# Performance work log

Hardware: AMD Instinct MI355X
Metric: run time of the kernel (lower is better)

The kernel has to match this reference:

```python
import jax, jax.numpy as jnp
import numpy as np

B, S, C, D, V = 64, 128, 32, 512, 20000

def setup_inputs() -> dict:
    key = jax.random.key(0)
    ks = jax.random.split(key, 16)
    sc = 1.0 / np.sqrt(D)
    emb = jax.random.normal(ks[0], (V + 1, D), jnp.float32) * 0.02
    emb = emb.at[V].set(0.0)  # padding_idx=-1 -> last row zero
    inp = dict(
        emb=emb,
        W_all_w=jax.random.uniform(ks[1], (4 * D, D), jnp.float32, -sc, sc),
        W_all_b=jnp.zeros((4 * D,), jnp.float32),
        U_all_w=jax.random.uniform(ks[2], (4 * D, D), jnp.float32, -sc, sc),
        U_all_b=jnp.zeros((4 * D,), jnp.float32),
        W_d_w=jax.random.uniform(ks[3], (D, D), jnp.float32, -sc, sc),
        W_d_b=jnp.zeros((D,), jnp.float32),
        sel_w=jax.random.uniform(ks[4], (64, 1), jnp.float32, -1.0, 1.0),
        sel_b=jnp.zeros((64,), jnp.float32),
        time_w=jax.random.uniform(ks[5], (D, 64), jnp.float32, -0.125, 0.125),
        time_b=jnp.zeros((D,), jnp.float32),
        out_w=jax.random.uniform(ks[6], (2, D), jnp.float32, -sc, sc),
        out_b=jnp.zeros((2,), jnp.float32),
        seq_time_step=jax.random.uniform(ks[7], (B, S), jnp.float32, 0.0, 365.0),
        input_seqs=jax.random.randint(ks[8], (B, S, C), 0, V),
        mask=jnp.zeros((B, S), bool),
        lengths=jax.random.randint(ks[9], (B,), 1, S),
        codemask=jnp.zeros((B, S, C), bool),
        label=jax.random.randint(ks[10], (B,), 0, 2),
    )
    return inp


def reference(emb, W_all_w, W_all_b, U_all_w, U_all_b, W_d_w, W_d_b,
              sel_w, sel_b, time_w, time_b, out_w, out_b, seq_time_step,
              input_seqs, mask, lengths, codemask, label):
    # visit embedding: sum code embeddings -> [B,S,D]
    x = emb[input_seqs].sum(axis=2)
    # time feature: 1 - tanh(selection_layer(t/180)^2) -> time_layer -> [B,S,D]
    t = (seq_time_step / 180.0)[..., None]                      # [B,S,1]
    tf = 1.0 - jnp.tanh(jnp.square(t * sel_w[:, 0] + sel_b))    # [B,S,64]
    tf = jnp.einsum('bsk,dk->bsd', tf, time_w) + time_b         # [B,S,D]
    # precompute input projection for all steps: [B,S,4D]
    ux = jnp.einsum('bsd,ed->bse', x, U_all_w) + U_all_b

    def step(carry, inputs):
        h, c = carry
        tf_s, ux_s = inputs                                      # [B,D], [B,4D]
        c_s1 = jnp.tanh(c @ W_d_w.T + W_d_b)
        c_adj = c - c_s1 + c_s1 * tf_s
        outs = h @ W_all_w.T + W_all_b + ux_s
        f, i, o, c_tmp = jnp.split(jax.nn.sigmoid(outs), 4, axis=1)
        c_new = f * c_adj + i * c_tmp
        h_new = o * jnp.tanh(c_new)
        return (h_new, c_new), h_new

    h0 = jnp.zeros((B, D), x.dtype)
    c0 = jnp.zeros((B, D), x.dtype)
    tf_t = jnp.swapaxes(tf, 0, 1)   # [S,B,D]
    ux_t = jnp.swapaxes(ux, 0, 1)   # [S,B,4D]
    _, hs = jax.lax.scan(step, (h0, c0), (tf_t, ux_t))
    outputs = jnp.swapaxes(hs, 0, 1)           # [B,S,D]
    pooled = outputs.max(axis=1)                # MaxPoolLayer without mask
    out = pooled @ out_w.T + out_b              # [B,2]
    return out
```

## Files before the change

### kernel.cpp

```cpp
#include <hip/hip_runtime.h>
#include <hip/hip_bf16.h>

#define B_ 64
#define S_ 128
#define C_ 32
#define D_ 512
#define V_ 20000

typedef float     f32x4  __attribute__((ext_vector_type(4)));
typedef _Float16  f16x8  __attribute__((ext_vector_type(8)));

#define AS1 __attribute__((address_space(1)))
#define AS3 __attribute__((address_space(3)))

#define OFF_XH   0ull
#define OFF_UH   8388608ull
#define OFF_AW   10485760ull
#define OFF_CB   13631488ull
#define OFF_PAD  13639680ull
#define OFF_TWT  13647872ull
#define OFF_EMBH 13778944ull
#define OFF_TF   34259968ull
#define OFF_UX   42648576ull
#define OFF_XB2  76203008ull

#define SENT32 0x7FFF7FFFu

__global__ void k_prep_fused(
    const float* __restrict__ outb, float* __restrict__ outv,
    int4* __restrict__ fillp,
    const float* __restrict__ Wallb, const float* __restrict__ Uallb,
    float* __restrict__ cb,
    const float* __restrict__ tw, float* __restrict__ twt,
    const float* __restrict__ U, _Float16* __restrict__ uh,
    const float* __restrict__ Wall, const float* __restrict__ Wd,
    int4* __restrict__ AW,
    const float* __restrict__ emb, _Float16* __restrict__ eh)
{
    const int blk = blockIdx.x;
    const int t   = threadIdx.x;
    if (blk < 1) {
        if (t < 128) outv[t] = outb[t & 1];
    } else if (blk < 4097) {
        fillp[(blk - 1) * 256 + t] =
            int4{(int)SENT32, (int)SENT32, (int)SENT32, (int)SENT32};
    } else if (blk < 4098) {
        #pragma unroll
        for (int k = 0; k < 8; k++) {
            int i = t * 8 + k;
            cb[i] = Wallb[i] + Uallb[i];
        }
    } else if (blk < 4130) {
        int i2 = (blk - 4098) * 256 + t;
        #pragma unroll
        for (int k = 0; k < 4; k++) {
            int i = i2 * 4 + k;
            twt[(i & 63) * 512 + (i >> 6)] = tw[i];
        }
    } else if (blk < 5154) {
        int i = (blk - 4130) * 256 + t;
        float4 v = ((const float4*)U)[i];
        union { _Float16 h[4]; unsigned long long u; } pk;
        pk.h[0] = (_Float16)v.x; pk.h[1] = (_Float16)v.y;
        pk.h[2] = (_Float16)v.z; pk.h[3] = (_Float16)v.w;
        ((unsigned long long*)uh)[i] = pk.u;
    } else if (blk < 5922) {
        int i = (blk - 5154) * 256 + t;
        int lane = i & 63;  int r = i >> 6;
        int kt = r & 15;    r >>= 4;
        int tile = r % 3;   r /= 3;
        int w = r & 7;      int m = r >> 3;
        int row16 = lane & 15, quad = lane >> 4;
        int q = tile * 2 + (row16 >> 3);
        int d = m * 64 + w * 8 + (row16 & 7);
        int k0 = kt * 32 + quad * 8;
        union { _Float16 h[8]; int4 v; } u;
        const float* src = nullptr;
        if (q < 4)       src = Wall + (size_t)(q * 512 + d) * 512 + k0;
        else if (q == 4) src = Wd   + (size_t)d * 512 + k0;
        #pragma unroll
        for (int j = 0; j < 8; j++) u.h[j] = src ? (_Float16)src[j] : (_Float16)0.f;
        AW[i] = u.v;
    } else {
        int i = (blk - 5922) * 256 + t;
        float2 v = ((const float2*)emb)[i];
        unsigned short hx = __builtin_bit_cast(unsigned short, (_Float16)v.x);
        unsigned short hy = __builtin_bit_cast(unsigned short, (_Float16)v.y);
        ((unsigned*)eh)[i] = (unsigned)hx | ((unsigned)hy << 16);
    }
}

__global__ void k_embed2(const _Float16* __restrict__ embh, const int* __restrict__ seqs,
                         _Float16* __restrict__ xh)
{
    int bs = blockIdx.x;
    int t  = threadIdx.x;
    __shared__ int rows[32];
    if (t < 32) {
        int r = seqs[(size_t)bs * C_ + t];
        rows[t] = (r < 0) ? V_ : r;
    }
    __syncthreads();
    float ax = 0.f, ay = 0.f;
    #pragma unroll 4
    for (int c = 0; c < C_; c++) {
        unsigned v = *(const unsigned*)(embh + (size_t)rows[c] * D_ + 2 * t);
        ax += (float)__builtin_bit_cast(_Float16, (unsigned short)v);
        ay += (float)__builtin_bit_cast(_Float16, (unsigned short)(v >> 16));
    }
    unsigned short hx = __builtin_bit_cast(unsigned short, (_Float16)ax);
    unsigned short hy = __builtin_bit_cast(unsigned short, (_Float16)ay);
    *(unsigned*)(xh + (size_t)bs * D_ + 2 * t) = (unsigned)hx | ((unsigned)hy << 16);
}

__global__ __launch_bounds__(512) void k_tf2(
    const float* __restrict__ stime, const float* __restrict__ selw,
    const float* __restrict__ selb, const float* __restrict__ twT,
    const float* __restrict__ timeb, _Float16* __restrict__ tf)
{
    int bb = blockIdx.x;
    int t  = threadIdx.x;
    __shared__ float s1[16][64];
    for (int idx = t; idx < 1024; idx += 512) {
        int bl = idx >> 6, j = idx & 63;
        float tv = stime[bb * 16 + bl] * (1.0f / 180.0f);
        float u  = tv * selw[j] + selb[j];
        s1[bl][j] = 1.0f - tanhf(u * u);
    }
    __syncthreads();
    int d = t;
    float acc[16];
    float tb = timeb[d];
    #pragma unroll
    for (int l = 0; l < 16; l++) acc[l] = tb;
    for (int j = 0; j < 64; j++) {
        float wj = twT[j * 512 + d];
        #pragma unroll
        for (int l = 0; l < 16; l++) acc[l] = fmaf(s1[l][j], wj, acc[l]);
    }
    #pragma unroll
    for (int l = 0; l < 16; l++)
        tf[(size_t)(bb * 16 + l) * 512 + d] = (_Float16)acc[l];
}

__device__ __forceinline__ void stage16(const _Float16* g, _Float16* l)
{
#if __has_builtin(__builtin_amdgcn_global_load_lds)
    __builtin_amdgcn_global_load_lds((const AS1 void*)g, (AS3 void*)l, 16, 0, 0);
#else
    *(int4*)l = *(const int4*)g;
#endif
}

__global__ __launch_bounds__(256, 4) void k_gemm3(const _Float16* __restrict__ A,
                                                  const _Float16* __restrict__ Bm,
                                                  _Float16* __restrict__ Cg)
{
    __shared__ __align__(16) _Float16 As[128 * 64];
    __shared__ __align__(16) _Float16 Bs[128 * 64];
    const int t = threadIdx.x;
    const int w = t >> 6, lane = t & 63;
    const int wm = w & 1, wn = w >> 1;
    const int m0 = blockIdx.y * 128, n0 = blockIdx.x * 128;
    const int r16 = lane & 15, quad = lane >> 4;

    const int srow = w * 8 + (lane >> 3);
    const int k8g  = (lane & 7) ^ ((lane >> 3) & 7);
    const _Float16* ga = A  + (size_t)(m0 + srow) * 512 + k8g * 8;
    const _Float16* gb = Bm + (size_t)(n0 + srow) * 512 + k8g * 8;
    _Float16* la = As + srow * 64 + (lane & 7) * 8;
    _Float16* lb = Bs + srow * 64 + (lane & 7) * 8;

    f32x4 acc[4][4] = {};
    for (int k0 = 0; k0 < 512; k0 += 64) {
        __syncthreads();
        #pragma unroll
        for (int r = 0; r < 4; r++) {
            stage16(ga + k0 + (size_t)r * 32 * 512, la + r * 32 * 64);
            stage16(gb + k0 + (size_t)r * 32 * 512, lb + r * 32 * 64);
        }
        __syncthreads();
        #pragma unroll
        for (int sub = 0; sub < 2; sub++) {
            f16x8 af[4], bf[4];
            const int ksl = ((sub * 4 + quad) ^ (r16 & 7)) * 8;
            #pragma unroll
            for (int i = 0; i < 4; i++) {
                af[i] = *(const f16x8*)(As + (wm * 64 + i * 16 + r16) * 64 + ksl);
                bf[i] = *(const f16x8*)(Bs + (wn * 64 + i * 16 + r16) * 64 + ksl);
            }
            #pragma unroll
            for (int i = 0; i < 4; i++)
                #pragma unroll
                for (int j = 0; j < 4; j++)
                    acc[i][j] = __builtin_amdgcn_mfma_f32_16x16x32_f16(
                                    af[i], bf[j], acc[i][j], 0, 0, 0);
        }
    }
    #pragma unroll
    for (int i = 0; i < 4; i++)
        #pragma unroll
        for (int j = 0; j < 4; j++) {
            int row = m0 + wm * 64 + i * 16 + quad * 4;
            int col = n0 + wn * 64 + j * 16 + r16;
            _Float16* cp = Cg + (size_t)row * 2048 + col;
            #pragma unroll
            for (int rg = 0; rg < 4; rg++)
                cp[(size_t)rg * 2048] = (_Float16)acc[i][j][rg];
        }
}

__device__ __forceinline__ float fsigm(float x)
{
    return __builtin_amdgcn_rcpf(1.f + __expf(-x));
}
__device__ __forceinline__ float ftanh(float x)
{
    return 1.f - 2.f * __builtin_amdgcn_rcpf(1.f + __expf(2.f * x));
}

__global__ __launch_bounds__(512, 2) void k_rnn7(
    const int4* __restrict__ AW,
    const float* __restrict__ cbv, const float* __restrict__ wdb,
    const _Float16* __restrict__ ux, const _Float16* __restrict__ tf,
    const float* __restrict__ outw,
    float* __restrict__ out,
    unsigned long long* __restrict__ xb64)
{
    const int t    = threadIdx.x;
    const int gid  = blockIdx.x >> 3;
    const int m    = blockIdx.x & 7;
    const int b0   = gid * 2;
    const int w    = t >> 6;
    const int lane = t & 63;
    const int col  = lane & 15;
    const int quad = lane >> 4;

    int4 Af[48];
    {
        const int4* src = AW + (size_t)(m * 8 + w) * 3072;
        #pragma unroll
        for (int i = 0; i < 48; i++) Af[i] = src[i * 64 + lane];
    }

    __shared__ __align__(16) _Float16 xstg[4 * 544];
    __shared__ __align__(16) float cmat[8][4][48];
    __shared__ float pstg[2][64];

    const bool act = (lane < 16);
    const int  pb  = lane >> 3;
    const int  pj  = lane & 7;
    const int  dl  = w * 8 + pj;
    const int  d   = m * 64 + dl;

    float cbf = 0, cbi = 0, cbo = 0, cbc = 0, bdv = 0;
    if (act) {
        cbf = cbv[d]; cbi = cbv[512 + d]; cbo = cbv[1024 + d]; cbc = cbv[1536 + d];
        bdv = wdb[d];
    }
    float c_reg = 0.f, pool = -1e30f;
    const int dw = w * 64 + lane;

    for (int s = 0; s < S_; s++) {
        float uf = 0, ui = 0, uo = 0, uc = 0, tv = 0;
        if (act) {
            size_t bs = (size_t)(b0 + pb) * S_ + s;
            const _Float16* up = ux + bs * 2048 + d;
            uf = (float)up[0];    ui = (float)up[512];
            uo = (float)up[1024]; uc = (float)up[1536];
            tv = (float)tf[bs * 512 + d];
        }

        unsigned long long val = 0ull;
        if (s > 0) {
            const unsigned long long* src =
                xb64 + (((size_t)s * 32 + gid) * 8 + w) * 64 + lane;
            int tries = 0;
            for (;;) {
                val = __hip_atomic_load(src, __ATOMIC_RELAXED,
                                        __HIP_MEMORY_SCOPE_AGENT);
                if ((unsigned)val != SENT32 && (unsigned)(val >> 32) != SENT32)
                    break;
                if (++tries > (1 << 22)) break;
            }
        }
        __syncthreads();
        xstg[0 * 544 + dw] = __builtin_bit_cast(_Float16, (unsigned short)(val));
        xstg[2 * 544 + dw] = __builtin_bit_cast(_Float16, (unsigned short)(val >> 16));
        xstg[1 * 544 + dw] = __builtin_bit_cast(_Float16, (unsigned short)(val >> 32));
        xstg[3 * 544 + dw] = __builtin_bit_cast(_Float16, (unsigned short)(val >> 48));
        __syncthreads();

        f32x4 a0 = {0, 0, 0, 0}, a1 = {0, 0, 0, 0}, a2 = {0, 0, 0, 0};
        #pragma unroll
        for (int kt = 0; kt < 16; kt++) {
            f16x8 b = {};
            if (col < 4)
                b = *(const f16x8*)(xstg + col * 544 + kt * 32 + quad * 8);
            a0 = __builtin_amdgcn_mfma_f32_16x16x32_f16(
                     __builtin_bit_cast(f16x8, Af[kt]),      b, a0, 0, 0, 0);
            a1 = __builtin_amdgcn_mfma_f32_16x16x32_f16(
                     __builtin_bit_cast(f16x8, Af[16 + kt]), b, a1, 0, 0, 0);
            a2 = __builtin_amdgcn_mfma_f32_16x16x32_f16(
                     __builtin_bit_cast(f16x8, Af[32 + kt]), b, a2, 0, 0, 0);
        }

        if (col < 4) {
            *(f32x4*)&cmat[w][col][ 0 + quad * 4] = a0;
            *(f32x4*)&cmat[w][col][16 + quad * 4] = a1;
            *(f32x4*)&cmat[w][col][32 + quad * 4] = a2;
        }

        if (act) {
            float f_  = cmat[w][pb][ 0 + pj];
            float i_  = cmat[w][pb][ 8 + pj];
            float o_  = cmat[w][pb][16 + pj];
            float g_  = cmat[w][pb][24 + pj];
            float wd_ = cmat[w][2 + pb][32 + pj];
            float gf = fsigm(f_ + cbf + uf);
            float gi = fsigm(i_ + cbi + ui);
            float go = fsigm(o_ + cbo + uo);
            float gc = fsigm(g_ + cbc + uc);
            float cs1  = ftanh(wd_ + bdv);
            float cadj = c_reg - cs1 + cs1 * tv;
            float cn   = gf * cadj + gi * gc;
            float hn   = go * ftanh(cn);
            c_reg = cn;
            pool  = fmaxf(pool, hn);
            unsigned hh = __builtin_bit_cast(unsigned short, (_Float16)hn);
            unsigned cc = __builtin_bit_cast(unsigned short, (_Float16)cn);
            unsigned pk = hh | (cc << 16);
            unsigned other = __shfl(pk, lane + 8);
            if (pb == 0 && s != S_ - 1) {
                unsigned long long ov =
                    (unsigned long long)pk | ((unsigned long long)other << 32);
                unsigned long long* dst =
                    xb64 + (((size_t)(s + 1) * 32 + gid) * 8 + m) * 64 + dl;
                __hip_atomic_store(dst, ov, __ATOMIC_RELAXED,
                                   __HIP_MEMORY_SCOPE_AGENT);
            }
        }
    }

    if (act) pstg[pb][dl] = pool;
    __syncthreads();
    if (t < 128) {
        int b = t >> 6, l = t & 63;
        float pv = pstg[b][l];
        int dg = m * 64 + l;
        float p0 = pv * outw[dg], p1 = pv * outw[512 + dg];
        #pragma unroll
        for (int off = 32; off > 0; off >>= 1) {
            p0 += __shfl_down(p0, off);
            p1 += __shfl_down(p1, off);
        }
        if (l == 0) {
            atomicAdd(&out[2 * (b0 + b)],     p0);
            atomicAdd(&out[2 * (b0 + b) + 1], p1);
        }
    }
}

extern "C" void kernel_launch(void* const* d_in, const int* in_sizes, int n_in,
                              void* d_out, int out_size, void* d_ws, size_t ws_size,
                              hipStream_t stream)
{
    const float* emb   = (const float*)d_in[0];
    const float* Wall  = (const float*)d_in[1];
    const float* Wallb = (const float*)d_in[2];
    const float* Uall  = (const float*)d_in[3];
    const float* Uallb = (const float*)d_in[4];
    const float* Wdw   = (const float*)d_in[5];
    const float* Wdb   = (const float*)d_in[6];
    const float* selw  = (const float*)d_in[7];
    const float* selb  = (const float*)d_in[8];
    const float* timew = (const float*)d_in[9];
    const float* timeb = (const float*)d_in[10];
    const float* outw  = (const float*)d_in[11];
    const float* outb  = (const float*)d_in[12];
    const float* stime = (const float*)d_in[13];
    const int*   seqs  = (const int*)d_in[14];
    float* out = (float*)d_out;
    char*  ws  = (char*)d_ws;

    _Float16* xh   = (_Float16*)(ws + OFF_XH);
    _Float16* uh   = (_Float16*)(ws + OFF_UH);
    int4*     aw   = (int4*)(ws + OFF_AW);
    float*    cbp  = (float*)(ws + OFF_CB);
    float*    twt  = (float*)(ws + OFF_TWT);
    _Float16* eh   = (_Float16*)(ws + OFF_EMBH);
    _Float16* tfp  = (_Float16*)(ws + OFF_TF);
    _Float16* uxp  = (_Float16*)(ws + OFF_UX);
    unsigned long long* xb = (unsigned long long*)(ws + OFF_XB2);

    k_prep_fused<<<25923, 256, 0, stream>>>(
        outb, out, (int4*)(ws + OFF_XB2),
        Wallb, Uallb, cbp,
        timew, twt,
        Uall, uh,
        Wall, Wdw, aw,
        emb, eh);
    k_embed2 <<<B_ * S_, 256, 0, stream>>>(eh, seqs, xh);
    k_tf2    <<<512,     512, 0, stream>>>(stime, selw, selb, twt, timeb, tfp);
    k_gemm3  <<<dim3(16, 64), 256, 0, stream>>>(xh, uh, uxp);
    k_rnn7   <<<256,     512, 0, stream>>>(aw, cbp, Wdb, uxp, tfp, outw, out, xb);
}
```

Measured before the change: 471.1 us.

## Interleave two independent batch pairs per RNN block to hide cross-block latency

Each recurrent block now handles four batch rows as two independent pairs, alternating phases between them, so one pair's MFMA and gate work can proceed while the other pair's hidden state from peer blocks is still in flight. The grid is halved to 128 blocks, and the exchange buffer is reindexed per pair. This targets the spin-wait latency of the cross-block handoff, at the cost of twice as many serial phases per block and fewer resident blocks.

```diff
diff --git a/kernel.cpp b/kernel.cpp
--- a/kernel.cpp
+++ b/kernel.cpp
@@ -219,7 +219,7 @@
     return 1.f - 2.f * __builtin_amdgcn_rcpf(1.f + __expf(2.f * x));
 }
 
-__global__ __launch_bounds__(512, 2) void k_rnn7(
+__global__ __launch_bounds__(512, 2) void k_rnn8(
     const int4* __restrict__ AW,
     const float* __restrict__ cbv, const float* __restrict__ wdb,
     const _Float16* __restrict__ ux, const _Float16* __restrict__ tf,
@@ -230,7 +230,7 @@
     const int t    = threadIdx.x;
     const int gid  = blockIdx.x >> 3;
     const int m    = blockIdx.x & 7;
-    const int b0   = gid * 2;
+    const int b0   = gid * 4;
     const int w    = t >> 6;
     const int lane = t & 63;
     const int col  = lane & 15;
@@ -243,9 +243,9 @@
         for (int i = 0; i < 48; i++) Af[i] = src[i * 64 + lane];
     }
 
-    __shared__ __align__(16) _Float16 xstg[4 * 544];
+    __shared__ __align__(16) _Float16 xstg[2][4 * 544];
     __shared__ __align__(16) float cmat[8][4][48];
-    __shared__ float pstg[2][64];
+    __shared__ float pstg[4][64];
 
     const bool act = (lane < 16);
     const int  pb  = lane >> 3;
@@ -258,13 +258,17 @@
         cbf = cbv[d]; cbi = cbv[512 + d]; cbo = cbv[1024 + d]; cbc = cbv[1536 + d];
         bdv = wdb[d];
     }
-    float c_reg = 0.f, pool = -1e30f;
+    float c_reg[2] = {0.f, 0.f};
+    float pool[2]  = {-1e30f, -1e30f};
     const int dw = w * 64 + lane;
 
-    for (int s = 0; s < S_; s++) {
+    for (int ph = 0; ph < 2 * S_; ph++) {
+        const int pair = ph & 1;
+        const int s    = ph >> 1;
+
         float uf = 0, ui = 0, uo = 0, uc = 0, tv = 0;
         if (act) {
-            size_t bs = (size_t)(b0 + pb) * S_ + s;
+            size_t bs = (size_t)(b0 + pair * 2 + pb) * S_ + s;
             const _Float16* up = ux + bs * 2048 + d;
             uf = (float)up[0];    ui = (float)up[512];
             uo = (float)up[1024]; uc = (float)up[1536];
@@ -274,7 +278,7 @@
         unsigned long long val = 0ull;
         if (s > 0) {
             const unsigned long long* src =
-                xb64 + (((size_t)s * 32 + gid) * 8 + w) * 64 + lane;
+                xb64 + ((((size_t)s * 2 + pair) * 16 + gid) * 8 + w) * 64 + lane;
             int tries = 0;
             for (;;) {
                 val = __hip_atomic_load(src, __ATOMIC_RELAXED,
@@ -285,24 +289,30 @@
             }
         }
         __syncthreads();
-        xstg[0 * 544 + dw] = __builtin_bit_cast(_Float16, (unsigned short)(val));
-        xstg[2 * 544 + dw] = __builtin_bit_cast(_Float16, (unsigned short)(val >> 16));
-        xstg[1 * 544 + dw] = __builtin_bit_cast(_Float16, (unsigned short)(val >> 32));
-        xstg[3 * 544 + dw] = __builtin_bit_cast(_Float16, (unsigned short)(val >> 48));
+        {
+            _Float16* xs = xstg[pair];
+            xs[0 * 544 + dw] = __builtin_bit_cast(_Float16, (unsigned short)(val));
+            xs[2 * 544 + dw] = __builtin_bit_cast(_Float16, (unsigned short)(val >> 16));
+            xs[1 * 544 + dw] = __builtin_bit_cast(_Float16, (unsigned short)(val >> 32));
+            xs[3 * 544 + dw] = __builtin_bit_cast(_Float16, (unsigned short)(val >> 48));
+        }
         __syncthreads();
 
         f32x4 a0 = {0, 0, 0, 0}, a1 = {0, 0, 0, 0}, a2 = {0, 0, 0, 0};
-        #pragma unroll
-        for (int kt = 0; kt < 16; kt++) {
-            f16x8 b = {};
-            if (col < 4)
-                b = *(const f16x8*)(xstg + col * 544 + kt * 32 + quad * 8);
-            a0 = __builtin_amdgcn_mfma_f32_16x16x32_f16(
-                     __builtin_bit_cast(f16x8, Af[kt]),      b, a0, 0, 0, 0);
-            a1 = __builtin_amdgcn_mfma_f32_16x16x32_f16(
-                     __builtin_bit_cast(f16x8, Af[16 + kt]), b, a1, 0, 0, 0);
-            a2 = __builtin_amdgcn_mfma_f32_16x16x32_f16(
-                     __builtin_bit_cast(f16x8, Af[32 + kt]), b, a2, 0, 0, 0);
+        {
+            const _Float16* xs = xstg[pair];
+            #pragma unroll
+            for (int kt = 0; kt < 16; kt++) {
+                f16x8 b = {};
+                if (col < 4)
+                    b = *(const f16x8*)(xs + col * 544 + kt * 32 + quad * 8);
+                a0 = __builtin_amdgcn_mfma_f32_16x16x32_f16(
+                         __builtin_bit_cast(f16x8, Af[kt]),      b, a0, 0, 0, 0);
+                a1 = __builtin_amdgcn_mfma_f32_16x16x32_f16(
+                         __builtin_bit_cast(f16x8, Af[16 + kt]), b, a1, 0, 0, 0);
+                a2 = __builtin_amdgcn_mfma_f32_16x16x32_f16(
+                         __builtin_bit_cast(f16x8, Af[32 + kt]), b, a2, 0, 0, 0);
+            }
         }
 
         if (col < 4) {
@@ -322,11 +332,11 @@
             float go = fsigm(o_ + cbo + uo);
             float gc = fsigm(g_ + cbc + uc);
             float cs1  = ftanh(wd_ + bdv);
-            float cadj = c_reg - cs1 + cs1 * tv;
+            float cadj = c_reg[pair] - cs1 + cs1 * tv;
             float cn   = gf * cadj + gi * gc;
             float hn   = go * ftanh(cn);
-            c_reg = cn;
-            pool  = fmaxf(pool, hn);
+            c_reg[pair] = cn;
+            pool[pair]  = fmaxf(pool[pair], hn);
             unsigned hh = __builtin_bit_cast(unsigned short, (_Float16)hn);
             unsigned cc = __builtin_bit_cast(unsigned short, (_Float16)cn);
             unsigned pk = hh | (cc << 16);
@@ -335,16 +345,16 @@
                 unsigned long long ov =
                     (unsigned long long)pk | ((unsigned long long)other << 32);
                 unsigned long long* dst =
-                    xb64 + (((size_t)(s + 1) * 32 + gid) * 8 + m) * 64 + dl;
+                    xb64 + ((((size_t)(s + 1) * 2 + pair) * 16 + gid) * 8 + m) * 64 + dl;
                 __hip_atomic_store(dst, ov, __ATOMIC_RELAXED,
                                    __HIP_MEMORY_SCOPE_AGENT);
             }
         }
     }
 
-    if (act) pstg[pb][dl] = pool;
+    if (act) { pstg[0 + pb][dl] = pool[0]; pstg[2 + pb][dl] = pool[1]; }
     __syncthreads();
-    if (t < 128) {
+    if (t < 256) {
         int b = t >> 6, l = t & 63;
         float pv = pstg[b][l];
         int dg = m * 64 + l;
@@ -403,5 +413,5 @@
     k_embed2 <<<B_ * S_, 256, 0, stream>>>(eh, seqs, xh);
     k_tf2    <<<512,     512, 0, stream>>>(stime, selw, selb, twt, timeb, tfp);
     k_gemm3  <<<dim3(16, 64), 256, 0, stream>>>(xh, uh, uxp);
-    k_rnn7   <<<256,     512, 0, stream>>>(aw, cbp, Wdb, uxp, tfp, outw, out, xb);
-}
+    k_rnn8   <<<128,     512, 0, stream>>>(aw, cbp, Wdb, uxp, tfp, outw, out, xb);
+}
```

Measured after the change: 748.6 us. 1.59x slower.
